# Optimization experiments

Measured on AMD Instinct MI355X. Metric: run time of the kernel, lower is better.

## Reference

```python
import jax, jax.numpy as jnp
import numpy as np

B, T, V, E, H = 4096, 16, 512, 512, 1024


def setup_inputs() -> dict:
    key = jax.random.key(0)
    ks = jax.random.split(key, 8)
    s = 0.05  # weight init scale
    return {
        "encoded_input": jax.random.normal(ks[0], (B, H), jnp.float32),
        "target": jax.random.randint(ks[1], (B, T), 0, V, jnp.int32),
        "emb": jax.random.normal(ks[2], (V, E), jnp.float32) * s,
        "W_ih": jax.random.normal(ks[3], (4 * H, E), jnp.float32) * s,
        "W_hh": jax.random.normal(ks[4], (4 * H, H), jnp.float32) * s,
        "b_ih": jax.random.normal(ks[5], (4 * H,), jnp.float32) * s,
        "b_hh": jax.random.normal(ks[6], (4 * H,), jnp.float32) * s,
        "W_out": jax.random.normal(ks[7], (V, H), jnp.float32) * s,
    }


def reference(encoded_input, target, emb, W_ih, W_hh, b_ih, b_hh, W_out):
    # Teacher-forced char LSTM decoder. Dropout(0.1) is identity in eval mode.
    b, t = target.shape
    # input char ids: start token 0, then shifted targets
    inp_ids = jnp.concatenate(
        [jnp.zeros((b, 1), target.dtype), target[:, :-1]], axis=1)  # [B,T]
    x = emb[inp_ids]  # [B,T,E]
    # precompute input contribution to gates for all steps
    xg = jnp.einsum('bte,ge->btg', x, W_ih) + b_ih + b_hh  # [B,T,4H]

    def step(carry, xs):
        h, c = carry
        xg_t, tgt_t = xs  # [B,4H], [B]
        gates = xg_t + h @ W_hh.T  # [B,4H]
        i, f, g, o = jnp.split(gates, 4, axis=-1)  # torch order i,f,g,o
        i = jax.nn.sigmoid(i)
        f = jax.nn.sigmoid(f)
        g = jnp.tanh(g)
        o = jax.nn.sigmoid(o)
        c = f * c + i * g
        h = o * jnp.tanh(c)
        logits = h @ W_out.T  # [B,V]
        # NLL of log_softmax at target index, expressed stably
        lse = jax.nn.logsumexp(logits, axis=-1)
        tgt_logit = jnp.take_along_axis(logits, tgt_t[:, None], axis=1)[:, 0]
        loss_t = lse - tgt_logit  # [B]
        return (h, c), loss_t

    h0 = encoded_input  # hidden = (encoded, encoded) for 1 layer
    (_, _), losses = jax.lax.scan(
        step, (h0, h0),
        (jnp.swapaxes(xg, 0, 1), target.T))  # scan over time: [T,B,...]
    return losses.sum(axis=0) / t  # [B] per-example mean loss
```

## Files before the change

kernel.cpp:

```cpp
#include <hip/hip_runtime.h>
#include <hip/hip_bf16.h>
#include <stdint.h>

typedef __attribute__((ext_vector_type(8))) short bf16x8;
typedef __attribute__((ext_vector_type(4))) float f32x4;

#define DEV __device__ __forceinline__
#define MFMA16(a, b, c) __builtin_amdgcn_mfma_f32_16x16x32_bf16(a, b, c, 0, 0, 0)

static constexpr int Bn = 4096;
static constexpr int Tn = 16;
static constexpr int Vn = 512;
static constexpr int En = 512;
static constexpr int Hn = 1024;
static constexpr int G4 = 4096;

DEV unsigned short f2bf(float f) {
    union { float f; uint32_t u; } v; v.f = f;
    return (unsigned short)((v.u + 0x7fffu + ((v.u >> 16) & 1u)) >> 16);
}
DEV float bf2f(unsigned short h) {
    union { uint32_t u; float f; } v; v.u = (uint32_t)h << 16; return v.f;
}
DEV float sigmoidf_(float x) { return 1.f / (1.f + __expf(-x)); }
DEV float tanhf_(float x)    { return 1.f - 2.f / (1.f + __expf(2.f * x)); }

DEV bf16x8 cvt8(const float* p) {
    f32x4 a = *(const f32x4*)p;
    f32x4 b = *(const f32x4*)(p + 4);
    bf16x8 o;
    o[0] = (short)f2bf(a[0]); o[1] = (short)f2bf(a[1]);
    o[2] = (short)f2bf(a[2]); o[3] = (short)f2bf(a[3]);
    o[4] = (short)f2bf(b[0]); o[5] = (short)f2bf(b[1]);
    o[6] = (short)f2bf(b[2]); o[7] = (short)f2bf(b[3]);
    return o;
}

#define GLOAD16(s, d) __builtin_amdgcn_global_load_lds( \
    (const __attribute__((address_space(1))) uint32_t*)(s), \
    (__attribute__((address_space(3))) uint32_t*)(d), 16, 0, 0)

__launch_bounds__(512, 2)
__global__ void lstm8(const unsigned short* __restrict__ Whp8,
                      const unsigned short* __restrict__ Hin,
                      const float* __restrict__ EGb,
                      const int* __restrict__ target, int t,
                      float* __restrict__ CstF,
                      unsigned short* __restrict__ Hout)
{
    __shared__ __align__(16) unsigned short lds[65536];

    const int tid = threadIdx.x;
    const int l   = tid & 63;
    const int w   = tid >> 6;
    const int wm  = w >> 2, wn = w & 3;
    const int q   = l >> 4, c15 = l & 15;
    const int bx  = blockIdx.x, by = blockIdx.y;
    const int n0  = bx * 256;
    const int U0  = by * 64;

    const int cB    = (((l & 7) ^ (l >> 3)) << 3);
    const int sw0   = ((q ^ (c15 & 7)) << 3);
    const int offA0 = c15 * 64 + sw0;
    const int offB0 = ((wn & 1) * 64 + c15) * 64 + sw0;

    int ids[4];
#pragma unroll
    for (int j = 0; j < 4; j++)
        ids[j] = (t > 0)
            ? target[(size_t)(n0 + wn * 64 + j * 16 + c15) * Tn + (t - 1)] : 0;

    f32x4 acc[8][4];
#pragma unroll
    for (int i = 0; i < 8; i++)
#pragma unroll
        for (int j = 0; j < 4; j++) acc[i][j] = f32x4{0.f, 0.f, 0.f, 0.f};

    auto stA = [&](int kts, int cbuf) {
        const unsigned short* page =
            Whp8 + (((size_t)(by * 16 + kts) * 2) << 13);
#pragma unroll
        for (int h = 0; h < 2; h++)
#pragma unroll
            for (int L = 0; L < 2; L++)
                GLOAD16(page + h * 8192 + L * 4096 + w * 512 + l * 8,
                        &lds[cbuf * 16384 + h * 8192 + L * 4096 + w * 512]);
    };
    auto stB = [&](int kts, int cbuf) {
#pragma unroll
        for (int h = 0; h < 2; h++)
#pragma unroll
            for (int L = 0; L < 2; L++)
                GLOAD16(Hin + (size_t)(n0 + h * 128 + L * 64 + w * 8 + (l >> 3)) * Hn
                            + kts * 64 + cB,
                        &lds[32768 + cbuf * 16384 + h * 8192 + L * 4096 + w * 512]);
    };

    stA(0, 0); stB(0, 0);
    stA(1, 1); stB(1, 1);
    asm volatile("s_waitcnt vmcnt(8)" ::: "memory");
    __builtin_amdgcn_s_barrier();

#pragma unroll 2
    for (int kt = 0; kt < 16; kt++) {
        const int cur = kt & 1;
        const unsigned short* Ab = &lds[cur * 16384 + wm * 8192];
        const unsigned short* Bb = &lds[32768 + cur * 16384 + (wn >> 1) * 8192];
        bf16x8 aF[8], bF[4];

#pragma unroll
        for (int i = 0; i < 8; i++)
            aF[i] = *(const bf16x8*)&Ab[offA0 + i * 1024];
#pragma unroll
        for (int j = 0; j < 4; j++)
            bF[j] = *(const bf16x8*)&Bb[offB0 + j * 1024];
        __builtin_amdgcn_s_setprio(1);
#pragma unroll
        for (int i = 0; i < 8; i++)
#pragma unroll
            for (int j = 0; j < 4; j++)
                acc[i][j] = MFMA16(aF[i], bF[j], acc[i][j]);
        __builtin_amdgcn_s_setprio(0);

#pragma unroll
        for (int i = 0; i < 8; i++)
            aF[i] = *(const bf16x8*)&Ab[(offA0 ^ 32) + i * 1024];
#pragma unroll
        for (int j = 0; j < 4; j++)
            bF[j] = *(const bf16x8*)&Bb[(offB0 ^ 32) + j * 1024];
        __builtin_amdgcn_s_setprio(1);
#pragma unroll
        for (int i = 0; i < 8; i++)
#pragma unroll
            for (int j = 0; j < 4; j++)
                acc[i][j] = MFMA16(aF[i], bF[j], acc[i][j]);
        __builtin_amdgcn_s_setprio(0);
        __builtin_amdgcn_s_barrier();

        const int kts = (kt + 2 < 16) ? (kt + 2) : 15;
        stA(kts, cur);
        stB(kts, cur);
        asm volatile("s_waitcnt vmcnt(8)" ::: "memory");
        __builtin_amdgcn_s_barrier();
    }

    unsigned short* sH = &lds[32768];
#pragma unroll
    for (int i = 0; i < 8; i++) {
        const int Uloc = wm * 32 + i * 4 + q;
#pragma unroll
        for (int j = 0; j < 4; j++) {
            f32x4 eg = *(const f32x4*)&EGb[(size_t)ids[j] * G4 + (U0 + Uloc) * 4];
            float ig = sigmoidf_(acc[i][j][0] + eg[0]);
            float fg = sigmoidf_(acc[i][j][1] + eg[1]);
            float gg = tanhf_  (acc[i][j][2] + eg[2]);
            float og = sigmoidf_(acc[i][j][3] + eg[3]);
            const size_t cidx =
                ((((size_t)(by * 16 + bx) * 8 + w) * 32 + i * 4 + j) << 6) + l;
            float cOld = CstF[cidx];
            float cNew = fg * cOld + ig * gg;
            float h    = og * tanhf_(cNew);
            CstF[cidx] = cNew;
            const int bl = wn * 64 + j * 16 + c15;
            sH[bl * 64 + (Uloc ^ ((bl & 7) << 3))] = f2bf(h);
        }
    }
    __syncthreads();
    {
        const int row = tid >> 1;
        const int hs  = tid & 1;
        const int sx  = row & 7;
        size_t go = (size_t)(n0 + row) * Hn + U0 + hs * 32;
#pragma unroll
        for (int s = 0; s < 4; s++) {
            const int slog = hs * 4 + s;
            bf16x8 v = *(const bf16x8*)&sH[row * 64 + ((slog ^ sx) << 3)];
            *(bf16x8*)&Hout[go + s * 8] = v;
        }
    }
}

__launch_bounds__(512, 1)
__global__ void logits256(const unsigned short* __restrict__ A,
                          const unsigned short* __restrict__ Wob,
                          const int* __restrict__ target,
                          float* __restrict__ partS,
                          float* __restrict__ partT)
{
    __shared__ __align__(16) unsigned short lds[65536];
    __shared__ float redS[4 * 256];
    __shared__ float redT[4 * 256];
    __shared__ int   tgL[256];

    const int tid = threadIdx.x;
    const int l   = tid & 63;
    const int w   = tid >> 6;
    const int wm  = w >> 2, wn = w & 3;
    const int q   = l >> 4, c15 = l & 15;
    const int bid = blockIdx.x;
    const int rb  = bid & 255, cb = bid >> 8;
    const int r0  = rb * 256;
    const int v0  = cb * 256;

    if (tid < 256) {
        int ra = r0 + tid;
        tgL[tid] = target[(size_t)(ra & (Bn - 1)) * Tn + (ra >> 12)];
    }

    const int cB    = (((l & 7) ^ (l >> 3)) << 3);
    const int sw0   = ((q ^ (c15 & 7)) << 3);
    const int offA0 = c15 * 64 + sw0;
    const int offB0 = ((wn & 1) * 64 + c15) * 64 + sw0;

    f32x4 acc[8][4];
#pragma unroll
    for (int i = 0; i < 8; i++)
#pragma unroll
        for (int j = 0; j < 4; j++) acc[i][j] = f32x4{0.f, 0.f, 0.f, 0.f};

    auto stA = [&](int kts, int cbuf) {
#pragma unroll
        for (int h = 0; h < 2; h++)
#pragma unroll
            for (int L = 0; L < 2; L++)
                GLOAD16(A + (size_t)(r0 + h * 128 + L * 64 + w * 8 + (l >> 3)) * Hn
                            + kts * 64 + cB,
                        &lds[cbuf * 16384 + h * 8192 + L * 4096 + w * 512]);
    };
    auto stB = [&](int kts, int cbuf) {
#pragma unroll
        for (int h = 0; h < 2; h++)
#pragma unroll
            for (int L = 0; L < 2; L++)
                GLOAD16(Wob + (size_t)(v0 + h * 128 + L * 64 + w * 8 + (l >> 3)) * Hn
                            + kts * 64 + cB,
                        &lds[32768 + cbuf * 16384 + h * 8192 + L * 4096 + w * 512]);
    };

    stA(0, 0); stB(0, 0);
    stA(1, 1); stB(1, 1);
    asm volatile("s_waitcnt vmcnt(8)" ::: "memory");
    __builtin_amdgcn_s_barrier();

#pragma unroll 2
    for (int kt = 0; kt < 16; kt++) {
        const int cur = kt & 1;
        const unsigned short* Ab = &lds[cur * 16384 + wm * 8192];
        const unsigned short* Bb = &lds[32768 + cur * 16384 + (wn >> 1) * 8192];
        bf16x8 aF[8], bF[4];

#pragma unroll
        for (int i = 0; i < 8; i++)
            aF[i] = *(const bf16x8*)&Ab[offA0 + i * 1024];
#pragma unroll
        for (int j = 0; j < 4; j++)
            bF[j] = *(const bf16x8*)&Bb[offB0 + j * 1024];
        __builtin_amdgcn_s_setprio(1);
#pragma unroll
        for (int i = 0; i < 8; i++)
#pragma unroll
            for (int j = 0; j < 4; j++)
                acc[i][j] = MFMA16(aF[i], bF[j], acc[i][j]);
        __builtin_amdgcn_s_setprio(0);

#pragma unroll
        for (int i = 0; i < 8; i++)
            aF[i] = *(const bf16x8*)&Ab[(offA0 ^ 32) + i * 1024];
#pragma unroll
        for (int j = 0; j < 4; j++)
            bF[j] = *(const bf16x8*)&Bb[(offB0 ^ 32) + j * 1024];
        __builtin_amdgcn_s_setprio(1);
#pragma unroll
        for (int i = 0; i < 8; i++)
#pragma unroll
            for (int j = 0; j < 4; j++)
                acc[i][j] = MFMA16(aF[i], bF[j], acc[i][j]);
        __builtin_amdgcn_s_setprio(0);
        __builtin_amdgcn_s_barrier();

        const int kts = (kt + 2 < 16) ? (kt + 2) : 15;
        stA(kts, cur);
        stB(kts, cur);
        asm volatile("s_waitcnt vmcnt(8)" ::: "memory");
        __builtin_amdgcn_s_barrier();
    }

#pragma unroll
    for (int i = 0; i < 8; i++)
#pragma unroll
        for (int rr = 0; rr < 4; rr++) {
            const int rloc = wm * 128 + i * 16 + q * 4 + rr;
            const int tg = tgL[rloc];
            float ps = 0.f, tv = 0.f;
#pragma unroll
            for (int j = 0; j < 4; j++) {
                float v = acc[i][j][rr];
                ps += __expf(v);
                int col = v0 + wn * 64 + j * 16 + c15;
                tv += (col == tg) ? v : 0.f;
            }
#pragma unroll
            for (int d = 1; d < 16; d <<= 1) {
                ps += __shfl_xor(ps, d);
                tv += __shfl_xor(tv, d);
            }
            if (c15 == 0) {
                redS[wn * 256 + rloc] = ps;
                redT[wn * 256 + rloc] = tv;
            }
        }
    __syncthreads();
    if (tid < 256) {
        float se = 0.f, tv = 0.f;
#pragma unroll
        for (int k = 0; k < 4; k++) {
            se += redS[k * 256 + tid];
            tv += redT[k * 256 + tid];
        }
        partS[(size_t)cb * (Bn * Tn) + r0 + tid] = se;
        partT[(size_t)cb * (Bn * Tn) + r0 + tid] = tv;
    }
}

template <int BM, int BN, int EPI>
__launch_bounds__(256, 2)
__global__ void gemm_k(const unsigned short* __restrict__ A, int lda,
                       const unsigned short* __restrict__ Bw, int ldb,
                       int K,
                       const float* __restrict__ biasp,
                       float* __restrict__ Out,
                       unsigned short* __restrict__ Outb, int ldo)
{
    constexpr int BK = 32;
    constexpr int WM = BM / 2, WN = BN / 2;
    constexpr int MI = WM / 16, NJ = WN / 16;

    __shared__ __align__(16) unsigned short sA[BM * BK];
    __shared__ __align__(16) unsigned short sB[BN * BK];

    const int tid = threadIdx.x;
    const int l   = tid & 63;
    const int w   = tid >> 6;
    const int wm  = w >> 1, wn = w & 1;
    const int m0  = blockIdx.y * BM;
    const int n0  = blockIdx.x * BN;

    f32x4 acc[MI][NJ];
#pragma unroll
    for (int i = 0; i < MI; i++)
#pragma unroll
        for (int j = 0; j < NJ; j++) acc[i][j] = f32x4{0.f, 0.f, 0.f, 0.f};

    const int srow = l >> 2;
    const int scol = (l & 3) * 8;
    const int q    = l >> 4;
    const int c15  = l & 15;

    for (int k0 = 0; k0 < K; k0 += BK) {
#pragma unroll
        for (int c = 0; c < BM / 64; c++)
            GLOAD16(A + (size_t)(m0 + c * 64 + w * 16 + srow) * lda + k0 + scol,
                    &sA[(c * 64 + w * 16) * BK]);
#pragma unroll
        for (int c = 0; c < BN / 64; c++)
            GLOAD16(Bw + (size_t)(n0 + c * 64 + w * 16 + srow) * ldb + k0 + scol,
                    &sB[(c * 64 + w * 16) * BK]);
        __syncthreads();

        bf16x8 aF[MI], bF[NJ];
#pragma unroll
        for (int i = 0; i < MI; i++)
            aF[i] = *(const bf16x8*)&sA[(wm * WM + i * 16 + c15) * BK + q * 8];
#pragma unroll
        for (int j = 0; j < NJ; j++)
            bF[j] = *(const bf16x8*)&sB[(wn * WN + j * 16 + c15) * BK + q * 8];
#pragma unroll
        for (int i = 0; i < MI; i++)
#pragma unroll
            for (int j = 0; j < NJ; j++)
                acc[i][j] = MFMA16(aF[i], bF[j], acc[i][j]);
        __syncthreads();
    }

#pragma unroll
    for (int j = 0; j < NJ; j++) {
        const int colp = n0 + wn * WN + j * 16 + c15;
        const float bj = biasp ? biasp[colp] : 0.f;
#pragma unroll
        for (int i = 0; i < MI; i++) {
            const size_t rb = (size_t)(m0 + wm * WM + i * 16 + 4 * q);
#pragma unroll
            for (int r = 0; r < 4; r++) {
                float vv = acc[i][j][r] + bj;
                if constexpr (EPI == 0) Out[(rb + r) * ldo + colp] = vv;
                else Outb[(rb + r) * ldo + colp] = f2bf(vv);
            }
        }
    }
}

__global__ void prep_all(const float* __restrict__ Wih,
                         const float* __restrict__ Whh,
                         const float* __restrict__ bih,
                         const float* __restrict__ bhh,
                         const float* __restrict__ Wout,
                         const float* __restrict__ emb,
                         unsigned short* __restrict__ Wihp,
                         unsigned short* __restrict__ Whp8,
                         float* __restrict__ biasp,
                         unsigned short* __restrict__ Wob,
                         unsigned short* __restrict__ embb)
{
    const int b = blockIdx.x;
    if (b < 1024) {
        int i = b * 256 + threadIdx.x;
        int n = i >> 6, kc = (i & 63) * 8;
        int g = n & 3, u = n >> 2;
        *(bf16x8*)&Wihp[(size_t)n * En + kc] =
            cvt8(Wih + (size_t)(g * Hn + u) * En + kc);
    } else if (b < 3072) {
        int idx = (b - 1024) * 256 + threadIdx.x;
        int o = idx * 8;
        int p = o & 8191;
        int h = (o >> 13) & 1;
        int kt = (o >> 14) & 15;
        int by = o >> 18;
        int r = p >> 6;
        int slot = (p & 63) >> 3;
        int cl = ((slot ^ (r & 7)) << 3);
        int n = by * 256 + h * 128 + r;
        int g = n & 3, u = n >> 2;
        *(bf16x8*)&Whp8[o] =
            cvt8(Whh + (size_t)(g * Hn + u) * Hn + kt * 64 + cl);
    } else if (b < 3088) {
        int n = (b - 3072) * 256 + threadIdx.x;
        int g = n & 3, u = n >> 2;
        biasp[n] = bih[g * Hn + u] + bhh[g * Hn + u];
    } else if (b < 3344) {
        int i = (b - 3088) * 256 + threadIdx.x;
        size_t off = (size_t)i * 8;
        *(bf16x8*)&Wob[off] = cvt8(Wout + off);
    } else {
        int i = (b - 3344) * 256 + threadIdx.x;
        size_t off = (size_t)i * 8;
        *(bf16x8*)&embb[off] = cvt8(emb + off);
    }
}

__global__ void init_state(const float* __restrict__ enc,
                           float* __restrict__ CstF,
                           unsigned short* __restrict__ Xh0,
                           float* __restrict__ loss)
{
    int f = blockIdx.x * 256 + threadIdx.x;
    int l = f & 63, q = l >> 4, c15 = l & 15;
    int ij = (f >> 6) & 31, i = ij >> 2, j = ij & 3;
    int w = (f >> 11) & 7, wm = w >> 2, wn = w & 3;
    int bx = (f >> 14) & 15, by = (f >> 18) & 15;
    int b = bx * 256 + wn * 64 + j * 16 + c15;
    int U = by * 64 + wm * 32 + i * 4 + q;
    CstF[f] = enc[(size_t)b * Hn + U];
    if (f < Bn * Hn / 8) {
        int m = f >> 7, u8 = (f & 127) * 8;
        *(bf16x8*)&Xh0[(size_t)m * Hn + u8] = cvt8(enc + (size_t)m * Hn + u8);
    }
    if (f < Bn) loss[f] = 0.f;
}

__global__ void lse_k(const unsigned short* __restrict__ lg,
                      const int* __restrict__ target, int t,
                      float* __restrict__ lossOut)
{
    int w = threadIdx.x >> 6, l = threadIdx.x & 63;
    int ra = blockIdx.x * 4 + w;
    const unsigned short* row = lg + (size_t)ra * Vn;
    bf16x8 v = *(const bf16x8*)&row[l * 8];
    float x0 = bf2f((unsigned short)v[0]), x1 = bf2f((unsigned short)v[1]);
    float x2 = bf2f((unsigned short)v[2]), x3 = bf2f((unsigned short)v[3]);
    float x4 = bf2f((unsigned short)v[4]), x5 = bf2f((unsigned short)v[5]);
    float x6 = bf2f((unsigned short)v[6]), x7 = bf2f((unsigned short)v[7]);
    float mx = fmaxf(fmaxf(fmaxf(x0, x1), fmaxf(x2, x3)),
                     fmaxf(fmaxf(x4, x5), fmaxf(x6, x7)));
#pragma unroll
    for (int d = 1; d < 64; d <<= 1) mx = fmaxf(mx, __shfl_xor(mx, d));
    float se = __expf(x0 - mx) + __expf(x1 - mx) + __expf(x2 - mx) +
               __expf(x3 - mx) + __expf(x4 - mx) + __expf(x5 - mx) +
               __expf(x6 - mx) + __expf(x7 - mx);
#pragma unroll
    for (int d = 1; d < 64; d <<= 1) se += __shfl_xor(se, d);
    if (l == 0) {
        int tg = target[(size_t)ra * Tn + t];
        lossOut[ra] += (mx + __logf(se)) - bf2f(row[tg]);
    }
}

__global__ void finalize_p(const float* __restrict__ partS,
                           const float* __restrict__ partT,
                           float* __restrict__ out)
{
    int m = blockIdx.x * 256 + threadIdx.x;
    float s = 0.f;
#pragma unroll
    for (int k = 0; k < 16; k++) {
        size_t ra = (size_t)k * Bn + m;
        float se = partS[ra] + partS[(size_t)(Bn * Tn) + ra];
        float tv = partT[ra] + partT[(size_t)(Bn * Tn) + ra];
        s += __logf(se) - tv;
    }
    out[m] = s * (1.f / 16.f);
}

__global__ void finalize_s(const float* __restrict__ loss,
                           float* __restrict__ out)
{
    int m = blockIdx.x * 256 + threadIdx.x;
    out[m] = loss[m] * (1.f / 16.f);
}

extern "C" void kernel_launch(void* const* d_in, const int* in_sizes, int n_in,
                              void* d_out, int out_size, void* d_ws, size_t ws_size,
                              hipStream_t stream)
{
    const float* enc    = (const float*)d_in[0];
    const int*   target = (const int*)d_in[1];
    const float* emb    = (const float*)d_in[2];
    const float* Wih    = (const float*)d_in[3];
    const float* Whh    = (const float*)d_in[4];
    const float* bih    = (const float*)d_in[5];
    const float* bhh    = (const float*)d_in[6];
    const float* Wout   = (const float*)d_in[7];
    float* out = (float*)d_out;
    (void)in_sizes; (void)n_in; (void)out_size;

    constexpr size_t SZ_Wihp  = (size_t)G4 * En * 2;
    constexpr size_t SZ_Whp8  = (size_t)G4 * Hn * 2;
    constexpr size_t SZ_Wob   = (size_t)Vn * Hn * 2;
    constexpr size_t SZ_biasp = (size_t)G4 * 4;
    constexpr size_t SZ_embb  = (size_t)Vn * En * 2;
    constexpr size_t SZ_EGb   = (size_t)Vn * G4 * 4;
    constexpr size_t SZ_Cst   = (size_t)Bn * Hn * 4;
    constexpr size_t SZ_H     = (size_t)Bn * Hn * 2;
    constexpr size_t SZ_LGS   = (size_t)Bn * Vn * 2;
    constexpr size_t SZ_PART  = (size_t)2 * Bn * Tn * 4;
    auto pad = [](size_t b) { return (b + 255) & ~(size_t)255; };
    const size_t fixed = pad(SZ_Wihp) + pad(SZ_Whp8) + pad(SZ_Wob) +
                         pad(SZ_biasp) + pad(SZ_embb) + pad(SZ_EGb) +
                         pad(SZ_Cst);
    const size_t needB = fixed + 17 * pad(SZ_H) + pad(SZ_LGS) +
                         2 * pad(SZ_PART);
    const bool batched = ws_size >= needB;

    size_t off = 0;
    char* base = (char*)d_ws;
    auto alloc = [&](size_t bytes) -> void* {
        void* p = base + off; off += pad(bytes); return p;
    };
    unsigned short* Wihp  = (unsigned short*)alloc(SZ_Wihp);
    unsigned short* Whp8  = (unsigned short*)alloc(SZ_Whp8);
    unsigned short* Wob   = (unsigned short*)alloc(SZ_Wob);
    float*          biasp = (float*)alloc(SZ_biasp);
    unsigned short* embb  = (unsigned short*)alloc(SZ_embb);
    float*          EGb   = (float*)alloc(SZ_EGb);
    float*          CstF  = (float*)alloc(SZ_Cst);
    const int nslot = batched ? 17 : 3;
    unsigned short* Hs    = (unsigned short*)alloc((size_t)nslot * pad(SZ_H));
    unsigned short* lgS   = (unsigned short*)alloc(SZ_LGS);
    float*          partS = (float*)alloc(SZ_PART);
    float*          partT = (float*)alloc(SZ_PART);
    const size_t HSLOT = pad(SZ_H) / 2;

    prep_all  <<<3472, 256, 0, stream>>>(Wih, Whh, bih, bhh, Wout, emb,
                                         Wihp, Whp8, biasp, Wob, embb);
    init_state<<<16384, 256, 0, stream>>>(enc, CstF, Hs, partS);

    gemm_k<128, 128, 0><<<dim3(32, 4), 256, 0, stream>>>(
        embb, En, Wihp, En, En, biasp, EGb, nullptr, G4);

    if (batched) {
        for (int t = 0; t < Tn; t++)
            lstm8<<<dim3(16, 16), 512, 0, stream>>>(
                Whp8, Hs + (size_t)t * HSLOT, EGb, target, t, CstF,
                Hs + (size_t)(t + 1) * HSLOT);
        logits256<<<512, 512, 0, stream>>>(
            Hs + HSLOT, Wob, target, partS, partT);
        finalize_p<<<16, 256, 0, stream>>>(partS, partT, out);
    } else {
        for (int t = 0; t < Tn; t++) {
            unsigned short* hIn  = Hs + (size_t)(t % 3) * HSLOT;
            unsigned short* hOut = Hs + (size_t)((t + 1) % 3) * HSLOT;
            lstm8<<<dim3(16, 16), 512, 0, stream>>>(
                Whp8, hIn, EGb, target, t, CstF, hOut);
            gemm_k<128, 64, 2><<<dim3(8, 32), 256, 0, stream>>>(
                hOut, Hn, Wob, Hn, Hn, nullptr, nullptr, lgS, Vn);
            lse_k<<<1024, 256, 0, stream>>>(lgS, target, t, partS);
        }
        finalize_s<<<16, 256, 0, stream>>>(partS, out);
    }
}
```

Before: 902.4 us.

## Split LSTM step tile across 16 waves with 1024-thread blocks

Doubles the lstm8 block to 1024 threads, so each of 16 waves computes a 4x4 MFMA sub-tile instead of 8x4 while the block still covers the same 64-unit by 256-batch tile. Global-to-LDS staging now uses one load per thread per half, and the cell-state layout in both lstm8 and init_state is remapped to match. The target-id load moves after the K loop. The goal is more waves per CU to hide memory and LDS latency, at the cost of a lower MFMA-to-LDS-read ratio per wave. The launch bound of (1024, 4) may also force a tight register cap and cause spills.

```diff
diff --git a/kernel.cpp b/kernel.cpp
--- a/kernel.cpp
+++ b/kernel.cpp
@@ -40,7 +40,7 @@
     (const __attribute__((address_space(1))) uint32_t*)(s), \
     (__attribute__((address_space(3))) uint32_t*)(d), 16, 0, 0)
 
-__launch_bounds__(512, 2)
+__launch_bounds__(1024, 4)
 __global__ void lstm8(const unsigned short* __restrict__ Whp8,
                       const unsigned short* __restrict__ Hin,
                       const float* __restrict__ EGb,
@@ -59,20 +59,14 @@
     const int n0  = bx * 256;
     const int U0  = by * 64;
 
-    const int cB    = (((l & 7) ^ (l >> 3)) << 3);
+    const int cBt = (((tid & 7) ^ ((tid >> 3) & 7)) << 3);
     const int sw0   = ((q ^ (c15 & 7)) << 3);
-    const int offA0 = c15 * 64 + sw0;
-    const int offB0 = ((wn & 1) * 64 + c15) * 64 + sw0;
-
-    int ids[4];
-#pragma unroll
-    for (int j = 0; j < 4; j++)
-        ids[j] = (t > 0)
-            ? target[(size_t)(n0 + wn * 64 + j * 16 + c15) * Tn + (t - 1)] : 0;
-
-    f32x4 acc[8][4];
-#pragma unroll
-    for (int i = 0; i < 8; i++)
+    const int offA0 = wm * 4096 + c15 * 64 + sw0;
+    const int offB0 = wn * 4096 + c15 * 64 + sw0;
+
+    f32x4 acc[4][4];
+#pragma unroll
+    for (int i = 0; i < 4; i++)
 #pragma unroll
         for (int j = 0; j < 4; j++) acc[i][j] = f32x4{0.f, 0.f, 0.f, 0.f};
 
@@ -81,56 +75,52 @@
             Whp8 + (((size_t)(by * 16 + kts) * 2) << 13);
 #pragma unroll
         for (int h = 0; h < 2; h++)
-#pragma unroll
-            for (int L = 0; L < 2; L++)
-                GLOAD16(page + h * 8192 + L * 4096 + w * 512 + l * 8,
-                        &lds[cbuf * 16384 + h * 8192 + L * 4096 + w * 512]);
+            GLOAD16(page + h * 8192 + tid * 8,
+                    &lds[cbuf * 16384 + h * 8192 + tid * 8]);
     };
     auto stB = [&](int kts, int cbuf) {
 #pragma unroll
         for (int h = 0; h < 2; h++)
-#pragma unroll
-            for (int L = 0; L < 2; L++)
-                GLOAD16(Hin + (size_t)(n0 + h * 128 + L * 64 + w * 8 + (l >> 3)) * Hn
-                            + kts * 64 + cB,
-                        &lds[32768 + cbuf * 16384 + h * 8192 + L * 4096 + w * 512]);
+            GLOAD16(Hin + (size_t)(n0 + h * 128 + (tid >> 3)) * Hn
+                        + kts * 64 + cBt,
+                    &lds[32768 + cbuf * 16384 + h * 8192 + tid * 8]);
     };
 
     stA(0, 0); stB(0, 0);
     stA(1, 1); stB(1, 1);
-    asm volatile("s_waitcnt vmcnt(8)" ::: "memory");
+    asm volatile("s_waitcnt vmcnt(4)" ::: "memory");
     __builtin_amdgcn_s_barrier();
 
 #pragma unroll 2
     for (int kt = 0; kt < 16; kt++) {
         const int cur = kt & 1;
-        const unsigned short* Ab = &lds[cur * 16384 + wm * 8192];
-        const unsigned short* Bb = &lds[32768 + cur * 16384 + (wn >> 1) * 8192];
-        bf16x8 aF[8], bF[4];
-
-#pragma unroll
-        for (int i = 0; i < 8; i++)
+        const unsigned short* Ab = &lds[cur * 16384];
+        const unsigned short* Bb = &lds[32768 + cur * 16384];
+        bf16x8 aF[4], bF[4];
+
+#pragma unroll
+        for (int i = 0; i < 4; i++)
             aF[i] = *(const bf16x8*)&Ab[offA0 + i * 1024];
 #pragma unroll
         for (int j = 0; j < 4; j++)
             bF[j] = *(const bf16x8*)&Bb[offB0 + j * 1024];
         __builtin_amdgcn_s_setprio(1);
 #pragma unroll
-        for (int i = 0; i < 8; i++)
+        for (int i = 0; i < 4; i++)
 #pragma unroll
             for (int j = 0; j < 4; j++)
                 acc[i][j] = MFMA16(aF[i], bF[j], acc[i][j]);
         __builtin_amdgcn_s_setprio(0);
 
 #pragma unroll
-        for (int i = 0; i < 8; i++)
+        for (int i = 0; i < 4; i++)
             aF[i] = *(const bf16x8*)&Ab[(offA0 ^ 32) + i * 1024];
 #pragma unroll
         for (int j = 0; j < 4; j++)
             bF[j] = *(const bf16x8*)&Bb[(offB0 ^ 32) + j * 1024];
         __builtin_amdgcn_s_setprio(1);
 #pragma unroll
-        for (int i = 0; i < 8; i++)
+        for (int i = 0; i < 4; i++)
 #pragma unroll
             for (int j = 0; j < 4; j++)
                 acc[i][j] = MFMA16(aF[i], bF[j], acc[i][j]);
@@ -140,14 +130,20 @@
         const int kts = (kt + 2 < 16) ? (kt + 2) : 15;
         stA(kts, cur);
         stB(kts, cur);
-        asm volatile("s_waitcnt vmcnt(8)" ::: "memory");
+        asm volatile("s_waitcnt vmcnt(4)" ::: "memory");
         __builtin_amdgcn_s_barrier();
     }
 
+    int ids[4];
+#pragma unroll
+    for (int j = 0; j < 4; j++)
+        ids[j] = (t > 0)
+            ? target[(size_t)(n0 + wn * 64 + j * 16 + c15) * Tn + (t - 1)] : 0;
+
     unsigned short* sH = &lds[32768];
 #pragma unroll
-    for (int i = 0; i < 8; i++) {
-        const int Uloc = wm * 32 + i * 4 + q;
+    for (int i = 0; i < 4; i++) {
+        const int Uloc = wm * 16 + i * 4 + q;
 #pragma unroll
         for (int j = 0; j < 4; j++) {
             f32x4 eg = *(const f32x4*)&EGb[(size_t)ids[j] * G4 + (U0 + Uloc) * 4];
@@ -156,7 +152,7 @@
             float gg = tanhf_  (acc[i][j][2] + eg[2]);
             float og = sigmoidf_(acc[i][j][3] + eg[3]);
             const size_t cidx =
-                ((((size_t)(by * 16 + bx) * 8 + w) * 32 + i * 4 + j) << 6) + l;
+                ((((size_t)(by * 16 + bx) * 16 + w) * 16 + i * 4 + j) << 6) + l;
             float cOld = CstF[cidx];
             float cNew = fg * cOld + ig * gg;
             float h    = og * tanhf_(cNew);
@@ -167,15 +163,14 @@
     }
     __syncthreads();
     {
-        const int row = tid >> 1;
-        const int hs  = tid & 1;
-        const int sx  = row & 7;
-        size_t go = (size_t)(n0 + row) * Hn + U0 + hs * 32;
-#pragma unroll
-        for (int s = 0; s < 4; s++) {
-            const int slog = hs * 4 + s;
-            bf16x8 v = *(const bf16x8*)&sH[row * 64 + ((slog ^ sx) << 3)];
-            *(bf16x8*)&Hout[go + s * 8] = v;
+        const int row  = tid >> 2;
+        const int part = tid & 3;
+        size_t go = (size_t)(n0 + row) * Hn + U0;
+#pragma unroll
+        for (int s = 0; s < 2; s++) {
+            const int slog = part * 2 + s;
+            bf16x8 v = *(const bf16x8*)&sH[row * 64 + ((slog ^ (row & 7)) << 3)];
+            *(bf16x8*)&Hout[go + slog * 8] = v;
         }
     }
 }
@@ -454,11 +449,11 @@
 {
     int f = blockIdx.x * 256 + threadIdx.x;
     int l = f & 63, q = l >> 4, c15 = l & 15;
-    int ij = (f >> 6) & 31, i = ij >> 2, j = ij & 3;
-    int w = (f >> 11) & 7, wm = w >> 2, wn = w & 3;
+    int ij = (f >> 6) & 15, i = ij >> 2, j = ij & 3;
+    int w = (f >> 10) & 15, wm = w >> 2, wn = w & 3;
     int bx = (f >> 14) & 15, by = (f >> 18) & 15;
     int b = bx * 256 + wn * 64 + j * 16 + c15;
-    int U = by * 64 + wm * 32 + i * 4 + q;
+    int U = by * 64 + wm * 16 + i * 4 + q;
     CstF[f] = enc[(size_t)b * Hn + U];
     if (f < Bn * Hn / 8) {
         int m = f >> 7, u8 = (f & 127) * 8;
@@ -578,7 +573,7 @@
 
     if (batched) {
         for (int t = 0; t < Tn; t++)
-            lstm8<<<dim3(16, 16), 512, 0, stream>>>(
+            lstm8<<<dim3(16, 16), 1024, 0, stream>>>(
                 Whp8, Hs + (size_t)t * HSLOT, EGb, target, t, CstF,
                 Hs + (size_t)(t + 1) * HSLOT);
         logits256<<<512, 512, 0, stream>>>(
@@ -588,7 +583,7 @@
         for (int t = 0; t < Tn; t++) {
             unsigned short* hIn  = Hs + (size_t)(t % 3) * HSLOT;
             unsigned short* hOut = Hs + (size_t)((t + 1) % 3) * HSLOT;
-            lstm8<<<dim3(16, 16), 512, 0, stream>>>(
+            lstm8<<<dim3(16, 16), 1024, 0, stream>>>(
                 Whp8, hIn, EGb, target, t, CstF, hOut);
             gemm_k<128, 64, 2><<<dim3(8, 32), 256, 0, stream>>>(
                 hOut, Hn, Wob, Hn, Hn, nullptr, nullptr, lgS, Vn);
```

New measurement: 858.7 us. 1.05x faster.
